# Kernel tuning notes

Measured on AMD Instinct MI355X. Metric: run time of the kernel, lower is better.

Reference implementation:

```python
import jax, jax.numpy as jnp
import numpy as np


def _rot_grids(group_order, ks, dtype):
    """Normalized sampling grids for each rotation (align_corners=False convention)."""
    k = jnp.arange(group_order, dtype=dtype)
    theta = 2.0 * jnp.pi * k / group_order                      # [G]
    c, s = jnp.cos(theta), jnp.sin(theta)
    # F.affine_grid base coords with align_corners=False: centers of pixels in [-1,1]
    lin = (jnp.arange(ks, dtype=dtype) + 0.5) * (2.0 / ks) - 1.0
    y, x = jnp.meshgrid(lin, lin, indexing='ij')                 # [ks,ks] each
    # theta rows: [cos, -sin, 0], [sin, cos, 0] applied to (x, y, 1)
    gx = c[:, None, None] * x - s[:, None, None] * y             # [G,ks,ks]
    gy = s[:, None, None] * x + c[:, None, None] * y             # [G,ks,ks]
    return gx, gy


def _grid_sample_bilinear_zeros(img, gx, gy):
    """Bilinear grid_sample, padding_mode='zeros', align_corners=False.
    img: [C,H,W]; gx,gy: [G,H,W] normalized coords. Returns [C,G,H,W]."""
    C, H, W = img.shape
    dt = img.dtype
    # unnormalize (align_corners=False)
    ix = ((gx + 1.0) * W - 1.0) * 0.5
    iy = ((gy + 1.0) * H - 1.0) * 0.5
    ix0 = jnp.floor(ix)
    iy0 = jnp.floor(iy)
    wx1 = (ix - ix0).astype(dt); wx0 = 1.0 - wx1
    wy1 = (iy - iy0).astype(dt); wy0 = 1.0 - wy1

    def gather(iyf, ixf):
        xi = ixf.astype(jnp.int32)
        yi = iyf.astype(jnp.int32)
        valid = ((xi >= 0) & (xi < W) & (yi >= 0) & (yi < H)).astype(dt)
        xi_c = jnp.clip(xi, 0, W - 1)
        yi_c = jnp.clip(yi, 0, H - 1)
        return img[:, yi_c, xi_c] * valid                        # [C,G,H,W]

    out = (gather(iy0, ix0) * (wy0 * wx0)
           + gather(iy0, ix0 + 1.0) * (wy0 * wx1)
           + gather(iy0 + 1.0, ix0) * (wy1 * wx0)
           + gather(iy0 + 1.0, ix0 + 1.0) * (wy1 * wx1))
    return out


def setup_inputs() -> dict:
    key = jax.random.key(0)
    out_ch, in_ch, ks = 512, 256, 9
    base_weight = jax.random.normal(key, (out_ch, in_ch, ks, ks), dtype=jnp.float32)
    return {"base_weight": base_weight, "group_order": 8}


def reference(base_weight, group_order):
    O, I, ks, _ = base_weight.shape
    img = base_weight.reshape(O * I, ks, ks)                     # [C,H,W]
    gx, gy = _rot_grids(group_order, ks, base_weight.dtype)      # [G,ks,ks]
    out = _grid_sample_bilinear_zeros(img, gx, gy)               # [C,G,ks,ks]
    # concat over rotations along dim 0 -> [G*O, I, ks, ks]
    out = out.reshape(O, I, group_order, ks, ks).transpose(2, 0, 1, 3, 4)
    return out.reshape(group_order * O, I, ks, ks)
```

## Files before the change

### kernel.cpp

```cpp
#include <hip/hip_runtime.h>
#include <math.h>


#define KS   9
#define NPIX 81
#define NC   64
#define BLOCK 256

__global__ void st_make_table(float* __restrict__ tab, int G) {
    int i = blockIdx.x * blockDim.x + threadIdx.x;
    if (i >= G * NPIX) return;
    int g = i / NPIX;
    int p = i - g * NPIX;
    int py = p / KS, px = p - py * KS;
    double theta = 6.283185307179586 * (double)g / (double)G;
    double cth = cos(theta), sth = sin(theta);
    double lx = ((double)px + 0.5) * (2.0 / KS) - 1.0;
    double ly = ((double)py + 0.5) * (2.0 / KS) - 1.0;
    double gx = cth * lx - sth * ly;
    double gy = sth * lx + cth * ly;
    double ix = ((gx + 1.0) * KS - 1.0) * 0.5;
    double iy = ((gy + 1.0) * KS - 1.0) * 0.5;
    double ix0 = floor(ix), iy0 = floor(iy);
    double fx = ix - ix0, fy = iy - iy0;
    int x0 = (int)ix0, y0 = (int)iy0;

    double wx0 = 1.0 - fx, wx1 = fx;
    double pw0, pw1; int xs;
    if (x0 >= 0 && x0 < KS - 1)      { xs = x0;     pw0 = wx0; pw1 = wx1; }
    else if (x0 == KS - 1)           { xs = KS - 2; pw0 = 0.0; pw1 = wx0; }
    else if (x0 == -1)               { xs = 0;      pw0 = wx1; pw1 = 0.0; }
    else                             { xs = 0;      pw0 = 0.0; pw1 = 0.0; }

    int yA = y0, yB = y0 + 1;
    double wyA = (yA >= 0 && yA < KS) ? (1.0 - fy) : 0.0;
    double wyB = (yB >= 0 && yB < KS) ? fy : 0.0;
    int yAc = yA < 0 ? 0 : (yA > KS - 1 ? KS - 1 : yA);
    int yBc = yB < 0 ? 0 : (yB > KS - 1 ? KS - 1 : yB);
    int offA = (yAc * KS + xs) * 4;
    int offB = (yBc * KS + xs) * 4;

    float4* e0 = (float4*)(tab + (size_t)i * 8);
    *e0 = make_float4((float)(wyA * pw0), (float)(wyA * pw1),
                      (float)(wyB * pw0), (float)(wyB * pw1));
    int4* e1 = (int4*)(tab + (size_t)i * 8 + 4);
    *e1 = make_int4(offA, offB, 0, 0);
}

__global__ __launch_bounds__(BLOCK, 8) void st_rotate(
        const float* __restrict__ in, const float* __restrict__ tab,
        float* __restrict__ out, int C, int G) {
    __shared__ __align__(16) float lin[NC * NPIX];
    const int t = threadIdx.x;
    const int c0 = blockIdx.x * NC;

    {
        const float4* src = (const float4*)(in + (size_t)c0 * NPIX);
        float4* dst = (float4*)lin;
#pragma unroll
        for (int j = 0; j < (NC * NPIX / 4 + BLOCK - 1) / BLOCK; ++j) {
            int idx = t + j * BLOCK;
            if (idx < NC * NPIX / 4) dst[idx] = src[idx];
        }
    }
    __syncthreads();

    if (t >= 3 * NPIX) return;
    const int c_local = t / NPIX;
    const int p = t - c_local * NPIX;
    const float4* tw = (const float4*)tab;
    const int4* ti = (const int4*)tab;

    float4 w = tw[(size_t)p * 2];
    int4  ob = ti[(size_t)p * 2 + 1];

    for (int g = 0; g < G; ++g) {
        float4 wn; int4 obn;
        if (g + 1 < G) {
            wn  = tw[(size_t)((g + 1) * NPIX + p) * 2];
            obn = ti[(size_t)((g + 1) * NPIX + p) * 2 + 1];
        }
        const char* lb = (const char*)lin + c_local * (NPIX * 4);
        float* og = out + ((size_t)g * C + c0) * NPIX + t;
#pragma unroll 3
        for (int k = 0; k < NC / 3; ++k) {
            float a0 = *(const float*)(lb + ob.x);
            float a1 = *(const float*)(lb + ob.x + 4);
            float b0 = *(const float*)(lb + ob.y);
            float b1 = *(const float*)(lb + ob.y + 4);
            *og = a0 * w.x + a1 * w.y + b0 * w.z + b1 * w.w;
            lb += 3 * NPIX * 4;
            og += 3 * NPIX;
        }
        if (c_local == 0) {
            float a0 = *(const float*)(lb + ob.x);
            float a1 = *(const float*)(lb + ob.x + 4);
            float b0 = *(const float*)(lb + ob.y);
            float b1 = *(const float*)(lb + ob.y + 4);
            *og = a0 * w.x + a1 * w.y + b0 * w.z + b1 * w.w;
        }
        w = wn; ob = obn;
    }
}

extern "C" void kernel_launch(void* const* d_in, const int* in_sizes, int n_in,
                              void* d_out, int out_size, void* d_ws, size_t ws_size,
                              hipStream_t stream) {
    const float* in = (const float*)d_in[0];
    float* out = (float*)d_out;
    float* tab = (float*)d_ws;
    const int C = in_sizes[0] / NPIX;
    const int G = out_size / in_sizes[0];
    const int ents = G * NPIX;
    st_make_table<<<(ents + 255) / 256, 256, 0, stream>>>(tab, G);
    st_rotate<<<C / NC, BLOCK, 0, stream>>>(in, tab, out, C, G);
}
```

Baseline: 387.2 us.

## Stage rotated outputs in double-buffered shared memory for vectorized float4 stores

Computed outputs for each rotation now go into a double-buffered shared-memory tile and are then copied to global memory with float4 stores by all 256 threads, replacing scalar stores from 243 threads. The channel tile per block is halved to 32 so that the input and two output buffers fit in LDS, which doubles the number of blocks. A __syncthreads per rotation is added and the input-load loop is simplified to a strided loop. The aim is to speed up the write-bound output stream, at the cost of extra LDS traffic and per-iteration barriers.

```diff
diff --git a/kernel.cpp b/kernel.cpp
--- a/kernel.cpp
+++ b/kernel.cpp
@@ -4,7 +4,7 @@
 
 #define KS   9
 #define NPIX 81
-#define NC   64
+#define NC   32
 #define BLOCK 256
 
 __global__ void st_make_table(float* __restrict__ tab, int G) {
@@ -51,54 +51,57 @@
         const float* __restrict__ in, const float* __restrict__ tab,
         float* __restrict__ out, int C, int G) {
     __shared__ __align__(16) float lin[NC * NPIX];
+    __shared__ __align__(16) float lout[2][NC * NPIX];
     const int t = threadIdx.x;
     const int c0 = blockIdx.x * NC;
 
     {
         const float4* src = (const float4*)(in + (size_t)c0 * NPIX);
         float4* dst = (float4*)lin;
-#pragma unroll
-        for (int j = 0; j < (NC * NPIX / 4 + BLOCK - 1) / BLOCK; ++j) {
-            int idx = t + j * BLOCK;
-            if (idx < NC * NPIX / 4) dst[idx] = src[idx];
-        }
+        for (int j = t; j < NC * NPIX / 4; j += BLOCK) dst[j] = src[j];
     }
     __syncthreads();
 
-    if (t >= 3 * NPIX) return;
-    const int c_local = t / NPIX;
-    const int p = t - c_local * NPIX;
+    const int  c_local = t / NPIX;
+    const int  p = t - c_local * NPIX;
+    const bool active = t < 3 * NPIX;
+
     const float4* tw = (const float4*)tab;
-    const int4* ti = (const int4*)tab;
-
-    float4 w = tw[(size_t)p * 2];
-    int4  ob = ti[(size_t)p * 2 + 1];
+    const int4*  ti = (const int4*)tab;
+    float4 w = make_float4(0.f, 0.f, 0.f, 0.f);
+    int4   ob = make_int4(0, 0, 0, 0);
+    if (active) { w = tw[(size_t)p * 2]; ob = ti[(size_t)p * 2 + 1]; }
 
     for (int g = 0; g < G; ++g) {
-        float4 wn; int4 obn;
-        if (g + 1 < G) {
+        float4 wn = w; int4 obn = ob;
+        if (active && g + 1 < G) {
             wn  = tw[(size_t)((g + 1) * NPIX + p) * 2];
             obn = ti[(size_t)((g + 1) * NPIX + p) * 2 + 1];
         }
-        const char* lb = (const char*)lin + c_local * (NPIX * 4);
-        float* og = out + ((size_t)g * C + c0) * NPIX + t;
-#pragma unroll 3
-        for (int k = 0; k < NC / 3; ++k) {
-            float a0 = *(const float*)(lb + ob.x);
-            float a1 = *(const float*)(lb + ob.x + 4);
-            float b0 = *(const float*)(lb + ob.y);
-            float b1 = *(const float*)(lb + ob.y + 4);
-            *og = a0 * w.x + a1 * w.y + b0 * w.z + b1 * w.w;
-            lb += 3 * NPIX * 4;
-            og += 3 * NPIX;
+
+        if (active) {
+            float* ot = &lout[g & 1][t];
+            const char* lb = (const char*)lin + c_local * (NPIX * 4);
+#pragma unroll
+            for (int k = 0; k < 11; ++k) {
+                if (c_local + 3 * k < NC) {
+                    float a0 = *(const float*)(lb + ob.x);
+                    float a1 = *(const float*)(lb + ob.x + 4);
+                    float b0 = *(const float*)(lb + ob.y);
+                    float b1 = *(const float*)(lb + ob.y + 4);
+                    ot[k * 3 * NPIX] = a0 * w.x + a1 * w.y + b0 * w.z + b1 * w.w;
+                }
+                lb += 3 * NPIX * 4;
+            }
         }
-        if (c_local == 0) {
-            float a0 = *(const float*)(lb + ob.x);
-            float a1 = *(const float*)(lb + ob.x + 4);
-            float b0 = *(const float*)(lb + ob.y);
-            float b1 = *(const float*)(lb + ob.y + 4);
-            *og = a0 * w.x + a1 * w.y + b0 * w.z + b1 * w.w;
+        __syncthreads();
+
+        {
+            const float4* s4 = (const float4*)lout[g & 1];
+            float4* d4 = (float4*)(out + ((size_t)g * C + c0) * NPIX);
+            for (int j = t; j < NC * NPIX / 4; j += BLOCK) d4[j] = s4[j];
         }
+
         w = wn; ob = obn;
     }
 }
```

Result: faster. 372.5 us (-3.8%).
